# Optimization experiments

Measured on AMD Instinct MI355X. Metric: run time of the kernel, lower is better.

Reference implementation:

```python
import jax, jax.numpy as jnp
import numpy as np

EPS = 1e-06
FP8_MAX = 448.0  # float8_e4m3fn max
T, H = 8192, 4096


def setup_inputs() -> dict:
    key = jax.random.key(0)
    ks = jax.random.split(key, 5)
    return {
        "hidden_states": jax.random.normal(ks[0], (T, H), dtype=jnp.float32),
        "norm_w": jax.random.uniform(ks[1], (4, H), dtype=jnp.float32),
        "w": jax.random.uniform(ks[2], (3, H, H), dtype=jnp.float32),
        "wscale": jax.random.uniform(ks[3], (3,), dtype=jnp.float32),
        "scale": jax.random.uniform(ks[4], (3,), dtype=jnp.float32),
    }


def _rmsnorm(x, g):
    var = jnp.mean(x * x, axis=-1, keepdims=True)
    return x * jax.lax.rsqrt(var + EPS) * g


def _fp8_quant(x, s):
    # static per-tensor quant: scale, clamp to fp8 range, cast to e4m3 and back
    q = jnp.clip(x / s, -FP8_MAX, FP8_MAX)
    return q.astype(jnp.float8_e4m3fn).astype(jnp.float32)


def _fp8_linear(x, wq, s_in, s_w):
    qx = _fp8_quant(x, s_in)
    return (qx @ wq) * (s_in * s_w)


def reference(hidden_states, norm_w, w, wscale, scale):
    # weight fp8 quantization (module stores weights already in fp8)
    wq = w.astype(jnp.float8_e4m3fn).astype(jnp.float32)  # [3,H,H]

    z = jax.nn.relu(hidden_states)
    x = resid = z  # all_reduce == identity on one device
    y = _rmsnorm(x, norm_w[0])

    z2 = _fp8_linear(y, wq[0], scale[0], wscale[0])
    x2 = z2 + resid
    resid = x2
    y2 = _rmsnorm(x2, norm_w[1])

    z3 = _fp8_linear(y2, wq[1], scale[1], wscale[1])
    x3 = z3 + resid
    resid = x3
    y3 = _rmsnorm(x3, norm_w[2])

    z4 = _fp8_linear(y3, wq[2], scale[2], wscale[2])
    x4 = z4 + resid
    y4 = _rmsnorm(x4, norm_w[3])
    return y4
```

## Files before the change

kernel.cpp:

```cpp
#include <hip/hip_runtime.h>

typedef float f32x4 __attribute__((ext_vector_type(4)));
typedef long  l2    __attribute__((ext_vector_type(2)));

#define T_DIM 8192
#define H_DIM 4096

__device__ __forceinline__ unsigned int pack_fp8x4(float a, float b, float c, float d) {
    int v = __builtin_amdgcn_cvt_pk_fp8_f32(a, b, 0, false);
    v = __builtin_amdgcn_cvt_pk_fp8_f32(c, d, v, true);
    return (unsigned int)v;
}


__global__ __launch_bounds__(256) void wquant_kernel(
    const float* __restrict__ w, unsigned char* __restrict__ wqT)
{
    const int l  = blockIdx.z;
    const int n0 = blockIdx.x * 64;
    const int k0 = blockIdx.y * 64;
    const int tid = threadIdx.x;
    __shared__ unsigned char tile[64][68];
    const float* wl = w + (size_t)l * H_DIM * H_DIM;
#pragma unroll
    for (int p = 0; p < 4; ++p) {
        int r = p * 16 + (tid >> 4);
        int c = (tid & 15) * 4;
        f32x4 v = *(const f32x4*)(wl + (size_t)(k0 + r) * H_DIM + n0 + c);
        *(unsigned int*)&tile[r][c] = pack_fp8x4(v[0], v[1], v[2], v[3]);
    }
    __syncthreads();
    const int nl = tid >> 2;
    const int g  = tid & 3;
    unsigned int words[4];
#pragma unroll
    for (int wi = 0; wi < 4; ++wi) {
        const int kbase = (wi >> 1) * 32 + g * 8 + (wi & 1) * 4;
        unsigned int a = 0;
#pragma unroll
        for (int b = 0; b < 4; ++b)
            a |= (unsigned int)tile[kbase + b][nl] << (8 * b);
        words[wi] = a;
    }
    unsigned char* op = wqT + ((size_t)l * H_DIM + n0 + nl) * H_DIM + k0 + g * 16;
    uint4 ov; ov.x = words[0]; ov.y = words[1]; ov.z = words[2]; ov.w = words[3];
    *(uint4*)op = ov;
}

template <int MODE>
__global__ __launch_bounds__(256) void row_kernel(
    const float* __restrict__ in,
    float* __restrict__ resid_out,
    void* __restrict__ out,
    const float* __restrict__ g,
    const float* __restrict__ scale_p)
{
    const int row = blockIdx.x;
    const int tid = threadIdx.x;
    const float* rin = in + (size_t)row * H_DIM;
    float x[16];
    float ss = 0.0f;
#pragma unroll
    for (int j = 0; j < 4; ++j) {
        const int base = (j * 256 + tid) * 4;
        f32x4 v = *(const f32x4*)(rin + base);
        f32x4 rv;
#pragma unroll
        for (int i = 0; i < 4; ++i) {
            float t = v[i];
            if (MODE == 0) t = fmaxf(t, 0.0f);
            x[j * 4 + i] = t;
            rv[i] = t;
            ss += t * t;
        }
        if (MODE == 0)
            *(f32x4*)(resid_out + (size_t)row * H_DIM + base) = rv;
    }
#pragma unroll
    for (int off = 32; off > 0; off >>= 1)
        ss += __shfl_down(ss, off, 64);
    __shared__ float red[4];
    if ((tid & 63) == 0) red[tid >> 6] = ss;
    __syncthreads();
    const float var  = (red[0] + red[1] + red[2] + red[3]) * (1.0f / (float)H_DIM);
    const float rinv = 1.0f / sqrtf(var + 1e-6f);

    if (MODE == 2) {
        float* ro = (float*)out + (size_t)row * H_DIM;
#pragma unroll
        for (int j = 0; j < 4; ++j) {
            const int base = (j * 256 + tid) * 4;
            f32x4 gv = *(const f32x4*)(g + base);
            f32x4 ov;
#pragma unroll
            for (int i = 0; i < 4; ++i) ov[i] = (x[j * 4 + i] * rinv) * gv[i];
            *(f32x4*)(ro + base) = ov;
        }
    } else {
        const float s = scale_p[0];
        unsigned int* qo = (unsigned int*)out + (size_t)row * (H_DIM / 4);
#pragma unroll
        for (int j = 0; j < 4; ++j) {
            const int base = (j * 256 + tid) * 4;
            f32x4 gv = *(const f32x4*)(g + base);
            float q[4];
#pragma unroll
            for (int i = 0; i < 4; ++i) {
                float y = (x[j * 4 + i] * rinv) * gv[i];
                y = y / s;
                q[i] = fminf(fmaxf(y, -448.0f), 448.0f);
            }
            const int W = j * 256 + tid;
            const int nw = (W >> 4) * 16 + ((W >> 1) & 3) * 4 + ((W >> 3) & 1) * 2 + (W & 1);
            qo[nw] = pack_fp8x4(q[0], q[1], q[2], q[3]);
        }
    }
}

__device__ __forceinline__ void stage_half(const unsigned char* gsrc, unsigned char* ldsdst) {
    __builtin_amdgcn_global_load_lds(
        (const __attribute__((address_space(1))) unsigned int*)gsrc,
        (__attribute__((address_space(3))) unsigned int*)ldsdst, 16, 0, 0);
}

#define VM4 asm volatile("s_waitcnt vmcnt(4)" ::: "memory")
#define VM0 asm volatile("s_waitcnt vmcnt(0)" ::: "memory")
#define VMN ((void)0)
#define BAR  __builtin_amdgcn_s_barrier()
#define LGKM do { asm volatile("s_waitcnt lgkmcnt(0)" ::: "memory"); \
                  __builtin_amdgcn_sched_barrier(0); } while (0)
#define PRIO1 __builtin_amdgcn_s_setprio(1)
#define PRIO0 __builtin_amdgcn_s_setprio(0)

#define LDSA(mh, j)  (*(const l2*)(lds + oC + wrA + ((mh) * 4 + (j)) * 1024 + fragoff))
#define LDSB(nh, n2) (*(const l2*)(lds + oC + wcB + ((nh) * 2 + (n2)) * 1024 + fragoff))

#define MFMACL(MB, NB, FB0, FB1) do {                                               \
    _Pragma("unroll")                                                               \
    for (int j = 0; j < 4; ++j) {                                                   \
        l2 fa = (j == 0 ? fa0 : j == 1 ? fa1 : j == 2 ? fa2 : fa3);                 \
        acc[(MB)+j][(NB)+0] = __builtin_amdgcn_mfma_f32_16x16x32_fp8_fp8(           \
            fa[0], FB0[0], acc[(MB)+j][(NB)+0], 0, 0, 0);                           \
        acc[(MB)+j][(NB)+0] = __builtin_amdgcn_mfma_f32_16x16x32_fp8_fp8(           \
            fa[1], FB0[1], acc[(MB)+j][(NB)+0], 0, 0, 0);                           \
        acc[(MB)+j][(NB)+1] = __builtin_amdgcn_mfma_f32_16x16x32_fp8_fp8(           \
            fa[0], FB1[0], acc[(MB)+j][(NB)+1], 0, 0, 0);                           \
        acc[(MB)+j][(NB)+1] = __builtin_amdgcn_mfma_f32_16x16x32_fp8_fp8(           \
            fa[1], FB1[1], acc[(MB)+j][(NB)+1], 0, 0, 0);                           \
    } } while (0)

#define TILE(STG, VMLAST) do {                                                      \
                                                   \
    fa0 = LDSA(0,0); fa1 = LDSA(0,1); fa2 = LDSA(0,2); fa3 = LDSA(0,3);             \
    fbA0 = LDSB(0,0); fbA1 = LDSB(0,1);                                             \
    if (STG) stage_half(pA + kt2, lds + oS + 0 + wave * 1024);                      \
    BAR; LGKM; PRIO1;                                                               \
    MFMACL(0, 0, fbA0, fbA1);                                                       \
    PRIO0; BAR;                                                                     \
                                                   \
    fbB0 = LDSB(1,0); fbB1 = LDSB(1,1);                                             \
    if (STG) stage_half(pAh + kt2, lds + oS + 8192 + wave * 1024);                  \
    BAR; LGKM; PRIO1;                                                               \
    MFMACL(0, 2, fbB0, fbB1);                                                       \
    PRIO0; BAR;                                                                     \
                                                   \
    fa0 = LDSA(1,0); fa1 = LDSA(1,1); fa2 = LDSA(1,2); fa3 = LDSA(1,3);             \
    if (STG) stage_half(pB + kt2, lds + oS + 16384 + wave * 1024);                  \
    BAR; LGKM; PRIO1;                                                               \
    MFMACL(4, 2, fbB0, fbB1);                                                       \
    PRIO0; BAR;                                                                     \
                                     \
    if (STG) stage_half(pBh + kt2, lds + oS + 24576 + wave * 1024);                 \
    VMLAST;                                                                         \
    BAR; PRIO1;                                                                     \
    MFMACL(4, 0, fbA0, fbA1);                                                       \
    PRIO0; BAR;                                                                     \
} while (0)

#define ROTATE do { unsigned tmpo = oC; oC = oN; oN = oS; oS = tmpo; } while (0)

__global__ __launch_bounds__(512, 2) void gemm_fp8_kernel(
    const unsigned char* __restrict__ A,
    const unsigned char* __restrict__ B,
    float* __restrict__ C,
    const float* __restrict__ s_in,
    const float* __restrict__ s_w)
{
    __shared__ unsigned char lds[98304];

    const float alpha = s_in[0] * s_w[0];

    const int b = blockIdx.x;
    const int local = b >> 3, chunk = b & 7;
    const int bm = (chunk & 3) * 8 + (local & 7);
    const int bn = (chunk >> 2) * 8 + (local >> 3);

    const int tid  = threadIdx.x;
    const int wave = tid >> 6;
    const int lane = tid & 63;
    const int wr   = wave >> 2;
    const int wc   = wave & 3;

    const int fragoff = (lane & 15) * 64 + (((lane >> 4) ^ ((lane >> 1) & 3)) << 4);
    const int wrA = wr * 8192;
    const int wcB = 16384 + wc * 4096;

    const int trow  = tid >> 2;
    const int tslot = (tid & 3) ^ ((tid >> 3) & 3);
    const unsigned char* pA  = A + (size_t)(bm * 256 + trow) * H_DIM + tslot * 16;
    const unsigned char* pAh = pA + (size_t)128 * H_DIM;
    const unsigned char* pB  = B + (size_t)(bn * 256 + trow) * H_DIM + tslot * 16;
    const unsigned char* pBh = pB + (size_t)128 * H_DIM;

    const f32x4 zero = {0.0f, 0.0f, 0.0f, 0.0f};
    f32x4 acc[8][4];
#pragma unroll
    for (int m = 0; m < 8; ++m)
#pragma unroll
        for (int n = 0; n < 4; ++n) acc[m][n] = zero;

    l2 fa0, fa1, fa2, fa3, fbA0, fbA1, fbB0, fbB1;
    unsigned oC = 0, oN = 32768, oS = 65536;

    stage_half(pA,       lds + 0     + wave * 1024);
    stage_half(pAh,      lds + 8192  + wave * 1024);
    stage_half(pB,       lds + 16384 + wave * 1024);
    stage_half(pBh,      lds + 24576 + wave * 1024);
    stage_half(pA  + 64, lds + 32768 + 0     + wave * 1024);
    stage_half(pAh + 64, lds + 32768 + 8192  + wave * 1024);
    stage_half(pB  + 64, lds + 32768 + 16384 + wave * 1024);
    stage_half(pBh + 64, lds + 32768 + 24576 + wave * 1024);
    VM4;
    BAR;

#pragma unroll 1
    for (int t = 0; t < 62; ++t) {
        const int kt2 = (t + 2) << 6;
        TILE(1, VM4);
        ROTATE;
    }
    {
        const int kt2 = 0;
        TILE(0, VM0);
        ROTATE;
    }
    {
        const int kt2 = 0;
        TILE(0, VMN);
    }

    const int col0 = bn * 256 + wc * 64 + (lane & 15);
    const int row0 = bm * 256 + wr * 128 + ((lane >> 4) << 2);
#pragma unroll
    for (int m = 0; m < 8; ++m) {
#pragma unroll
        for (int i = 0; i < 4; ++i) {
            float* cp = C + (size_t)(row0 + m * 16 + i) * H_DIM + col0;
#pragma unroll
            for (int n = 0; n < 4; ++n)
                cp[n * 16] = acc[m][n][i] * alpha + cp[n * 16];
        }
    }
}

extern "C" void kernel_launch(void* const* d_in, const int* in_sizes, int n_in,
                              void* d_out, int out_size, void* d_ws, size_t ws_size,
                              hipStream_t stream) {
    const float* h   = (const float*)d_in[0];
    const float* nw  = (const float*)d_in[1];
    const float* w   = (const float*)d_in[2];
    const float* wsc = (const float*)d_in[3];
    const float* sc  = (const float*)d_in[4];
    float* out = (float*)d_out;

    unsigned char* wqT = (unsigned char*)d_ws;
    unsigned char* qx  = wqT + (size_t)3 * H_DIM * H_DIM;
    float* resid = (float*)(qx + (size_t)T_DIM * H_DIM);

    const size_t WSTRIDE = (size_t)H_DIM * H_DIM;

    wquant_kernel<<<dim3(64, 64, 3), 256, 0, stream>>>(w, wqT);

    row_kernel<0><<<T_DIM, 256, 0, stream>>>(h, resid, qx, nw + 0 * H_DIM, sc + 0);
    gemm_fp8_kernel<<<512, 512, 0, stream>>>(qx, wqT + 0 * WSTRIDE, resid, sc + 0, wsc + 0);

    row_kernel<1><<<T_DIM, 256, 0, stream>>>(resid, nullptr, qx, nw + 1 * H_DIM, sc + 1);
    gemm_fp8_kernel<<<512, 512, 0, stream>>>(qx, wqT + 1 * WSTRIDE, resid, sc + 1, wsc + 1);

    row_kernel<1><<<T_DIM, 256, 0, stream>>>(resid, nullptr, qx, nw + 2 * H_DIM, sc + 2);
    gemm_fp8_kernel<<<512, 512, 0, stream>>>(qx, wqT + 2 * WSTRIDE, resid, sc + 2, wsc + 2);

    row_kernel<2><<<T_DIM, 256, 0, stream>>>(resid, nullptr, out, nw + 3 * H_DIM, nullptr);
}
```

Measured before the change: 808.5 us.

## Switch FP8 GEMM to 32x32x64 scaled MFMA with simpler per-iteration pipeline

Replaces the 16x16x32 fp8 MFMA inner loop with the gfx950 mfma_scale 32x32x64 instruction, using unit scales. The operand layout in the quantized activations and transposed weights changes to match the new fragment shape, and the LDS fragment offsets change with it. The four barrier-separated sub-phases per K-tile become one barrier per tile, where the fragments for the next tile are read after the MFMAs. The intent is higher MFMA throughput and fewer barriers and LDS reads, at the cost of changing the epilogue mapping and the sensitivity of the scheduling.

```diff
diff --git a/kernel.cpp b/kernel.cpp
--- a/kernel.cpp
+++ b/kernel.cpp
@@ -1,10 +1,13 @@
 #include <hip/hip_runtime.h>
 
-typedef float f32x4 __attribute__((ext_vector_type(4)));
-typedef long  l2    __attribute__((ext_vector_type(2)));
+typedef float f32x4  __attribute__((ext_vector_type(4)));
+typedef float f32x16 __attribute__((ext_vector_type(16)));
+typedef int   i32x4  __attribute__((ext_vector_type(4)));
+typedef int   i32x8  __attribute__((ext_vector_type(8)));
 
 #define T_DIM 8192
 #define H_DIM 4096
+#define SC1 0x7f7f7f7f
 
 __device__ __forceinline__ unsigned int pack_fp8x4(float a, float b, float c, float d) {
     int v = __builtin_amdgcn_cvt_pk_fp8_f32(a, b, 0, false);
@@ -35,11 +38,10 @@
     unsigned int words[4];
 #pragma unroll
     for (int wi = 0; wi < 4; ++wi) {
-        const int kbase = (wi >> 1) * 32 + g * 8 + (wi & 1) * 4;
         unsigned int a = 0;
 #pragma unroll
         for (int b = 0; b < 4; ++b)
-            a |= (unsigned int)tile[kbase + b][nl] << (8 * b);
+            a |= (unsigned int)tile[g * 16 + wi * 4 + b][nl] << (8 * b);
         words[wi] = a;
     }
     unsigned char* op = wqT + ((size_t)l * H_DIM + n0 + nl) * H_DIM + k0 + g * 16;
@@ -110,9 +112,7 @@
                 y = y / s;
                 q[i] = fminf(fmaxf(y, -448.0f), 448.0f);
             }
-            const int W = j * 256 + tid;
-            const int nw = (W >> 4) * 16 + ((W >> 1) & 3) * 4 + ((W >> 3) & 1) * 2 + (W & 1);
-            qo[nw] = pack_fp8x4(q[0], q[1], q[2], q[3]);
+            qo[j * 256 + tid] = pack_fp8x4(q[0], q[1], q[2], q[3]);
         }
     }
 }
@@ -125,59 +125,44 @@
 
 #define VM4 asm volatile("s_waitcnt vmcnt(4)" ::: "memory")
 #define VM0 asm volatile("s_waitcnt vmcnt(0)" ::: "memory")
-#define VMN ((void)0)
-#define BAR  __builtin_amdgcn_s_barrier()
-#define LGKM do { asm volatile("s_waitcnt lgkmcnt(0)" ::: "memory"); \
-                  __builtin_amdgcn_sched_barrier(0); } while (0)
-#define PRIO1 __builtin_amdgcn_s_setprio(1)
-#define PRIO0 __builtin_amdgcn_s_setprio(0)
-
-#define LDSA(mh, j)  (*(const l2*)(lds + oC + wrA + ((mh) * 4 + (j)) * 1024 + fragoff))
-#define LDSB(nh, n2) (*(const l2*)(lds + oC + wcB + ((nh) * 2 + (n2)) * 1024 + fragoff))
-
-#define MFMACL(MB, NB, FB0, FB1) do {                                               \
-    _Pragma("unroll")                                                               \
-    for (int j = 0; j < 4; ++j) {                                                   \
-        l2 fa = (j == 0 ? fa0 : j == 1 ? fa1 : j == 2 ? fa2 : fa3);                 \
-        acc[(MB)+j][(NB)+0] = __builtin_amdgcn_mfma_f32_16x16x32_fp8_fp8(           \
-            fa[0], FB0[0], acc[(MB)+j][(NB)+0], 0, 0, 0);                           \
-        acc[(MB)+j][(NB)+0] = __builtin_amdgcn_mfma_f32_16x16x32_fp8_fp8(           \
-            fa[1], FB0[1], acc[(MB)+j][(NB)+0], 0, 0, 0);                           \
-        acc[(MB)+j][(NB)+1] = __builtin_amdgcn_mfma_f32_16x16x32_fp8_fp8(           \
-            fa[0], FB1[0], acc[(MB)+j][(NB)+1], 0, 0, 0);                           \
-        acc[(MB)+j][(NB)+1] = __builtin_amdgcn_mfma_f32_16x16x32_fp8_fp8(           \
-            fa[1], FB1[1], acc[(MB)+j][(NB)+1], 0, 0, 0);                           \
+#define LGKM0 do { asm volatile("s_waitcnt lgkmcnt(0)" ::: "memory"); \
+                   __builtin_amdgcn_sched_barrier(0); } while (0)
+
+#define RD(OR) do {                                                               \
+    _Pragma("unroll") for (int m = 0; m < 4; ++m) {                               \
+        i32x4 lo = *(const i32x4*)(lds + (OR) + wrA + m * 2048 + fo0);            \
+        i32x4 hi = *(const i32x4*)(lds + (OR) + wrA + m * 2048 + fo1);            \
+        fa[m] = __builtin_shufflevector(lo, hi, 0,1,2,3,4,5,6,7);                 \
+    }                                                                             \
+    _Pragma("unroll") for (int n = 0; n < 2; ++n) {                               \
+        i32x4 lo = *(const i32x4*)(lds + (OR) + wcB + n * 2048 + fo0);            \
+        i32x4 hi = *(const i32x4*)(lds + (OR) + wcB + n * 2048 + fo1);            \
+        fb[n] = __builtin_shufflevector(lo, hi, 0,1,2,3,4,5,6,7);                 \
     } } while (0)
 
-#define TILE(STG, VMLAST) do {                                                      \
-                                                   \
-    fa0 = LDSA(0,0); fa1 = LDSA(0,1); fa2 = LDSA(0,2); fa3 = LDSA(0,3);             \
-    fbA0 = LDSB(0,0); fbA1 = LDSB(0,1);                                             \
-    if (STG) stage_half(pA + kt2, lds + oS + 0 + wave * 1024);                      \
-    BAR; LGKM; PRIO1;                                                               \
-    MFMACL(0, 0, fbA0, fbA1);                                                       \
-    PRIO0; BAR;                                                                     \
-                                                   \
-    fbB0 = LDSB(1,0); fbB1 = LDSB(1,1);                                             \
-    if (STG) stage_half(pAh + kt2, lds + oS + 8192 + wave * 1024);                  \
-    BAR; LGKM; PRIO1;                                                               \
-    MFMACL(0, 2, fbB0, fbB1);                                                       \
-    PRIO0; BAR;                                                                     \
-                                                   \
-    fa0 = LDSA(1,0); fa1 = LDSA(1,1); fa2 = LDSA(1,2); fa3 = LDSA(1,3);             \
-    if (STG) stage_half(pB + kt2, lds + oS + 16384 + wave * 1024);                  \
-    BAR; LGKM; PRIO1;                                                               \
-    MFMACL(4, 2, fbB0, fbB1);                                                       \
-    PRIO0; BAR;                                                                     \
-                                     \
-    if (STG) stage_half(pBh + kt2, lds + oS + 24576 + wave * 1024);                 \
-    VMLAST;                                                                         \
-    BAR; PRIO1;                                                                     \
-    MFMACL(4, 0, fbA0, fbA1);                                                       \
-    PRIO0; BAR;                                                                     \
+#define MM do {                                                                   \
+    __builtin_amdgcn_s_setprio(1);                                                \
+    _Pragma("unroll") for (int m = 0; m < 4; ++m)                                 \
+    _Pragma("unroll") for (int n = 0; n < 2; ++n)                                 \
+        acc[m][n] = __builtin_amdgcn_mfma_scale_f32_32x32x64_f8f6f4(              \
+            fa[m], fb[n], acc[m][n], 0, 0, 0, SC1, 0, SC1);                       \
+    __builtin_amdgcn_s_setprio(0);                                                \
 } while (0)
 
-#define ROTATE do { unsigned tmpo = oC; oC = oN; oN = oS; oS = tmpo; } while (0)
+#define ITER(STG, VMW, OR, OS) do {                                               \
+    if (STG) {                                                                    \
+        stage_half(pA  + kt2, lds + (OS) + 0     + wave * 1024);                  \
+        stage_half(pAh + kt2, lds + (OS) + 8192  + wave * 1024);                  \
+        stage_half(pB  + kt2, lds + (OS) + 16384 + wave * 1024);                  \
+        stage_half(pBh + kt2, lds + (OS) + 24576 + wave * 1024);                  \
+        kt2 += 64;                                                                \
+    }                                                                             \
+    VMW;                                                                          \
+    __builtin_amdgcn_s_barrier();                                                 \
+    MM;                                                                           \
+    RD(OR);                                                                       \
+    LGKM0;                                                                        \
+} while (0)
 
 __global__ __launch_bounds__(512, 2) void gemm_fp8_kernel(
     const unsigned char* __restrict__ A,
@@ -201,7 +186,9 @@
     const int wr   = wave >> 2;
     const int wc   = wave & 3;
 
-    const int fragoff = (lane & 15) * 64 + (((lane >> 4) ^ ((lane >> 1) & 3)) << 4);
+    const int sw  = (lane >> 1) & 3;
+    const int fo0 = (lane & 31) * 64 + ((((lane >> 5) * 2) + 0 ^ sw)) * 16;
+    const int fo1 = (lane & 31) * 64 + ((((lane >> 5) * 2) + 1 ^ sw)) * 16;
     const int wrA = wr * 8192;
     const int wcB = 16384 + wc * 4096;
 
@@ -212,15 +199,16 @@
     const unsigned char* pB  = B + (size_t)(bn * 256 + trow) * H_DIM + tslot * 16;
     const unsigned char* pBh = pB + (size_t)128 * H_DIM;
 
-    const f32x4 zero = {0.0f, 0.0f, 0.0f, 0.0f};
-    f32x4 acc[8][4];
-#pragma unroll
-    for (int m = 0; m < 8; ++m)
-#pragma unroll
-        for (int n = 0; n < 4; ++n) acc[m][n] = zero;
-
-    l2 fa0, fa1, fa2, fa3, fbA0, fbA1, fbB0, fbB1;
-    unsigned oC = 0, oN = 32768, oS = 65536;
+    f32x16 acc[4][2];
+#pragma unroll
+    for (int m = 0; m < 4; ++m)
+#pragma unroll
+        for (int n = 0; n < 2; ++n)
+#pragma unroll
+            for (int e = 0; e < 16; ++e) acc[m][n][e] = 0.0f;
+
+    i32x8 fa[4], fb[2];
+    int kt2;
 
     stage_half(pA,       lds + 0     + wave * 1024);
     stage_half(pAh,      lds + 8192  + wave * 1024);
@@ -231,34 +219,34 @@
     stage_half(pB  + 64, lds + 32768 + 16384 + wave * 1024);
     stage_half(pBh + 64, lds + 32768 + 24576 + wave * 1024);
     VM4;
-    BAR;
+    __builtin_amdgcn_s_barrier();
+    RD(0);
+    LGKM0;
+    kt2 = 128;
 
 #pragma unroll 1
-    for (int t = 0; t < 62; ++t) {
-        const int kt2 = (t + 2) << 6;
-        TILE(1, VM4);
-        ROTATE;
-    }
-    {
-        const int kt2 = 0;
-        TILE(0, VM0);
-        ROTATE;
-    }
-    {
-        const int kt2 = 0;
-        TILE(0, VMN);
-    }
-
-    const int col0 = bn * 256 + wc * 64 + (lane & 15);
-    const int row0 = bm * 256 + wr * 128 + ((lane >> 4) << 2);
-#pragma unroll
-    for (int m = 0; m < 8; ++m) {
-#pragma unroll
-        for (int i = 0; i < 4; ++i) {
-            float* cp = C + (size_t)(row0 + m * 16 + i) * H_DIM + col0;
-#pragma unroll
-            for (int n = 0; n < 4; ++n)
-                cp[n * 16] = acc[m][n][i] * alpha + cp[n * 16];
+    for (int t3 = 0; t3 < 60; t3 += 3) {
+        ITER(1, VM4, 32768, 65536);
+        ITER(1, VM4, 65536, 0);
+        ITER(1, VM4, 0,     32768);
+    }
+    ITER(1, VM4, 32768, 65536);
+    ITER(1, VM4, 65536, 0);
+    ITER(0, VM0, 0,     0);
+    MM;
+
+    const int lrow0 = bm * 256 + wr * 128 + 4 * (lane >> 5);
+    const int lcol0 = bn * 256 + wc * 64 + (lane & 31);
+#pragma unroll
+    for (int m = 0; m < 4; ++m) {
+#pragma unroll
+        for (int n = 0; n < 2; ++n) {
+#pragma unroll
+            for (int e = 0; e < 16; ++e) {
+                const int row = lrow0 + m * 32 + (e & 3) + 8 * (e >> 2);
+                float* cp = C + (size_t)row * H_DIM + lcol0 + n * 32;
+                *cp = acc[m][n][e] * alpha + *cp;
+            }
         }
     }
 }
```

After: 676.7 us. 16.3% less time.
